# Optimization experiments

Hardware: AMD Instinct MI355X
Metric: run time of the kernel (lower is better)

The kernel has to match this reference:

```python
import jax, jax.numpy as jnp
import numpy as np
import math

B, CIN, H, W = 8, 64, 64, 64
C = 64  # channels (== in_channels, required since conv_out is unused and residual is added raw)
TEMPERATURE = 1.0


def setup_inputs() -> dict:
    key = jax.random.key(0)
    ks = jax.random.split(key, 7)
    s = 1.0 / math.sqrt(CIN)
    return {
        "x": jax.random.normal(ks[0], (B, CIN, H, W), dtype=jnp.float32),
        "wq": jax.random.uniform(ks[1], (C, CIN), jnp.float32, -s, s),
        "bq": jax.random.uniform(ks[2], (C,), jnp.float32, -s, s),
        "wk": jax.random.uniform(ks[3], (C, CIN), jnp.float32, -s, s),
        "bk": jax.random.uniform(ks[4], (C,), jnp.float32, -s, s),
        "wv": jax.random.uniform(ks[5], (C, CIN), jnp.float32, -s, s),
        "bv": jax.random.uniform(ks[6], (C,), jnp.float32, -s, s),
    }


def reference(x, wq, bq, wk, bk, wv, bv):
    b, cin, h, w = x.shape
    n = h * w
    xf = x.reshape(b, cin, n)  # [B,Cin,N]
    # 1x1 convs == per-pixel GEMM
    q = jnp.einsum('oc,bcn->bon', wq, xf) + bq[None, :, None]  # [B,C,N]
    k = jnp.einsum('oc,bcn->bon', wk, xf) + bk[None, :, None]
    v = jnp.einsum('oc,bcn->bon', wv, xf) + bv[None, :, None]
    # 'channel' whitening: subtract per-channel spatial mean
    q_mean = q.mean(axis=2, keepdims=True)  # [B,C,1]
    k_mean = k.mean(axis=2, keepdims=True)
    q = q - q_mean
    k = k - k_mean
    scale = math.sqrt(C)
    # pairwise term: softmax over keys of whitened q.k / (scale*temperature)
    sim = jnp.einsum('bcn,bcm->bnm', q, k) / (scale * TEMPERATURE)  # [B,N,N]
    sim = jax.nn.softmax(sim, axis=2)
    out = jnp.einsum('bnm,bcm->bcn', sim, v)  # [B,C,N]
    # unary term: softmax(query_mean . key) over keys, no scaling (as in source)
    unary = jax.nn.softmax(jnp.einsum('bc,bcm->bm', q_mean[:, :, 0], k), axis=-1)  # [B,N]
    out_unary = jnp.einsum('bcm,bm->bc', v, unary)  # [B,C]
    out = out + out_unary[:, :, None]
    return x + out.reshape(b, C, h, w)
```

## Files before the change

### kernel.cpp

```cpp
#include <hip/hip_runtime.h>
#include <stdint.h>

#define N_PIX 4096
#define NB 8

typedef __attribute__((ext_vector_type(8))) short short8;
typedef __attribute__((ext_vector_type(4))) float f32x4;
typedef __attribute__((ext_vector_type(2))) uint32_t u32x2;

#define SCL 0.18033688011112042f
#define LOG2E 1.4426950408889634f

__device__ __forceinline__ short f2bf(float x){
  union { float f; uint32_t u; } a; a.f = x;
  uint32_t r = a.u + 0x7FFFu + ((a.u >> 16) & 1u);
  return (short)(r >> 16);
}
__device__ __forceinline__ float bf2f(short h){
  union { uint32_t u; float f; } a; a.u = ((uint32_t)(uint16_t)h) << 16; return a.f;
}
__device__ __forceinline__ uint32_t cvtpk(float lo, float hi){
  uint32_t r;
  asm("v_cvt_pk_bf16_f32 %0, %1, %2" : "=v"(r) : "v"(lo), "v"(hi));
  return r;
}
__device__ __forceinline__ float fexp2(float x){ return __builtin_amdgcn_exp2f(x); }
__device__ __forceinline__ float wredSum(float v){
  #pragma unroll
  for (int m = 1; m < 64; m <<= 1) v += __shfl_xor(v, m);
  return v;
}
__device__ __forceinline__ float wredMax(float v){
  #pragma unroll
  for (int m = 1; m < 64; m <<= 1) v = fmaxf(v, __shfl_xor(v, m));
  return v;
}

__global__ __launch_bounds__(256) void k_xmean(const float* __restrict__ x, float* __restrict__ xm){
  int row = blockIdx.x;
  int tid = threadIdx.x;
  const float* xr = x + (size_t)row * N_PIX;
  float s = 0.f;
  #pragma unroll
  for (int i = 0; i < 16; i++) s += xr[tid + 256*i];
  s = wredSum(s);
  __shared__ float red[4];
  if ((tid & 63) == 0) red[tid >> 6] = s;
  __syncthreads();
  if (tid == 0) xm[row] = (red[0]+red[1]+red[2]+red[3]) * (1.0f / N_PIX);
}

__global__ void k_means(const float* __restrict__ wq, const float* __restrict__ bq,
                        const float* __restrict__ wk, const float* __restrict__ bk,
                        const float* __restrict__ xm, float* __restrict__ qm, float* __restrict__ km){
  int b = blockIdx.x; int c = threadIdx.x;
  float sq = 0.f, sk = 0.f;
  for (int cc = 0; cc < 64; cc++){
    float xv = xm[b*64 + cc];
    sq += wq[c*64 + cc] * xv;
    sk += wk[c*64 + cc] * xv;
  }
  qm[b*64 + c] = sq + bq[c];
  km[b*64 + c] = sk + bk[c];
}

__global__ __launch_bounds__(256) void k_qkv(
    const float* __restrict__ x,
    const float* __restrict__ wq, const float* __restrict__ bq,
    const float* __restrict__ wk, const float* __restrict__ bk,
    const float* __restrict__ wv, const float* __restrict__ bv,
    const float* __restrict__ qm, const float* __restrict__ km,
    short* __restrict__ Q, short* __restrict__ Kf, short* __restrict__ Vf,
    float* __restrict__ u)
{
  int blk = blockIdx.x;
  int b  = blk >> 5;
  int n0 = (blk & 31) * 128;
  int tid = threadIdx.x;
  int w = tid >> 6, l = tid & 63, lr = l & 15, lg = l >> 4;
  const float* xb = x + (size_t)b * 64 * N_PIX;

  int ncol[2];
  ncol[0] = n0 + w*32 + lr;
  ncol[1] = ncol[0] + 16;

  short8 bx[2][2];
  #pragma unroll
  for (int tj = 0; tj < 2; tj++){
    #pragma unroll
    for (int kc = 0; kc < 2; kc++){
      short8 t;
      #pragma unroll
      for (int j = 0; j < 8; j++){
        int cp = kc*32 + lg*8 + j;
        t[j] = f2bf(xb[(size_t)cp * N_PIX + ncol[tj]]);
      }
      bx[tj][kc] = t;
    }
  }

  float qmv[4][4];
  #pragma unroll
  for (int ti = 0; ti < 4; ti++)
    #pragma unroll
    for (int r = 0; r < 4; r++)
      qmv[ti][r] = qm[b*64 + ti*16 + lg*4 + r];

  short* Qb  = Q  + (size_t)b * N_PIX * 64;
  short* Kfb = Kf + (size_t)b * N_PIX * 64;
  short* Vfb = Vf + (size_t)b * N_PIX * 64;
  const f32x4 z4 = {0.f, 0.f, 0.f, 0.f};

  {
    short8 aw[4][2];
    #pragma unroll
    for (int ti = 0; ti < 4; ti++)
      #pragma unroll
      for (int kc = 0; kc < 2; kc++){
        const float* wr = wq + (ti*16 + lr)*64 + kc*32 + lg*8;
        short8 t;
        #pragma unroll
        for (int j = 0; j < 8; j++) t[j] = f2bf(wr[j]);
        aw[ti][kc] = t;
      }
    f32x4 acc[4][2];
    #pragma unroll
    for (int ti = 0; ti < 4; ti++)
      #pragma unroll
      for (int tj = 0; tj < 2; tj++){
        acc[ti][tj] = z4;
        #pragma unroll
        for (int kc = 0; kc < 2; kc++)
          acc[ti][tj] = __builtin_amdgcn_mfma_f32_16x16x32_bf16(aw[ti][kc], bx[tj][kc], acc[ti][tj], 0, 0, 0);
      }
    float adj[4][4];
    #pragma unroll
    for (int ti = 0; ti < 4; ti++)
      #pragma unroll
      for (int r = 0; r < 4; r++)
        adj[ti][r] = bq[ti*16 + lg*4 + r] - qmv[ti][r];
    #pragma unroll
    for (int ti = 0; ti < 4; ti++)
      #pragma unroll
      for (int tj = 0; tj < 2; tj++){
        float v0 = (acc[ti][tj][0] + adj[ti][0]) * SCL;
        float v1 = (acc[ti][tj][1] + adj[ti][1]) * SCL;
        float v2 = (acc[ti][tj][2] + adj[ti][2]) * SCL;
        float v3 = (acc[ti][tj][3] + adj[ti][3]) * SCL;
        uint32_t p0 = ((uint32_t)(uint16_t)f2bf(v1) << 16) | (uint16_t)f2bf(v0);
        uint32_t p1 = ((uint32_t)(uint16_t)f2bf(v3) << 16) | (uint16_t)f2bf(v2);
        uint32_t* qr = (uint32_t*)(Qb + (size_t)ncol[tj]*64);
        qr[ti*8 + lg*2]     = p0;
        qr[ti*8 + lg*2 + 1] = p1;
      }
  }

  {
    short8 aw[4][2];
    #pragma unroll
    for (int ti = 0; ti < 4; ti++)
      #pragma unroll
      for (int kc = 0; kc < 2; kc++){
        const float* wr = wk + (ti*16 + lr)*64 + kc*32 + lg*8;
        short8 t;
        #pragma unroll
        for (int j = 0; j < 8; j++) t[j] = f2bf(wr[j]);
        aw[ti][kc] = t;
      }
    f32x4 acc[4][2];
    #pragma unroll
    for (int ti = 0; ti < 4; ti++)
      #pragma unroll
      for (int tj = 0; tj < 2; tj++){
        acc[ti][tj] = z4;
        #pragma unroll
        for (int kc = 0; kc < 2; kc++)
          acc[ti][tj] = __builtin_amdgcn_mfma_f32_16x16x32_bf16(aw[ti][kc], bx[tj][kc], acc[ti][tj], 0, 0, 0);
      }
    float adj[4][4];
    #pragma unroll
    for (int ti = 0; ti < 4; ti++)
      #pragma unroll
      for (int r = 0; r < 4; r++)
        adj[ti][r] = bk[ti*16 + lg*4 + r] - km[b*64 + ti*16 + lg*4 + r];
    float up[2] = {0.f, 0.f};
    #pragma unroll
    for (int ti = 0; ti < 4; ti++)
      #pragma unroll
      for (int tj = 0; tj < 2; tj++){
        float v0 = acc[ti][tj][0] + adj[ti][0];
        float v1 = acc[ti][tj][1] + adj[ti][1];
        float v2 = acc[ti][tj][2] + adj[ti][2];
        float v3 = acc[ti][tj][3] + adj[ti][3];
        up[tj] += qmv[ti][0]*v0 + qmv[ti][1]*v1 + qmv[ti][2]*v2 + qmv[ti][3]*v3;
        uint32_t p0 = ((uint32_t)(uint16_t)f2bf(v1) << 16) | (uint16_t)f2bf(v0);
        uint32_t p1 = ((uint32_t)(uint16_t)f2bf(v3) << 16) | (uint16_t)f2bf(v2);
        int n = ncol[tj];
        int di = (n >> 4)*512 + (ti >> 1)*256
               + ((n & 15) + 16*(2*(ti & 1) + (lg >> 1)))*4 + (lg & 1)*2;
        uint32_t* kr = (uint32_t*)Kfb;
        kr[di]     = p0;
        kr[di + 1] = p1;
      }
    #pragma unroll
    for (int tj = 0; tj < 2; tj++){
      float s = up[tj];
      s += __shfl_xor(s, 16);
      s += __shfl_xor(s, 32);
      if (lg == 0) u[(size_t)b*N_PIX + ncol[tj]] = s;
    }
  }

  {
    short8 aw[4][2];
    #pragma unroll
    for (int ti = 0; ti < 4; ti++)
      #pragma unroll
      for (int kc = 0; kc < 2; kc++){
        const float* wr = wv + (ti*16 + lr)*64 + kc*32 + lg*8;
        short8 t;
        #pragma unroll
        for (int j = 0; j < 8; j++) t[j] = f2bf(wr[j]);
        aw[ti][kc] = t;
      }
    f32x4 acc[4][2];
    #pragma unroll
    for (int ti = 0; ti < 4; ti++)
      #pragma unroll
      for (int tj = 0; tj < 2; tj++){
        acc[ti][tj] = z4;
        #pragma unroll
        for (int kc = 0; kc < 2; kc++)
          acc[ti][tj] = __builtin_amdgcn_mfma_f32_16x16x32_bf16(aw[ti][kc], bx[tj][kc], acc[ti][tj], 0, 0, 0);
      }
    #pragma unroll
    for (int ti = 0; ti < 4; ti++)
      #pragma unroll
      for (int tj = 0; tj < 2; tj++){
        int n = ncol[tj];
        short* vr = Vfb + (n >> 5)*2048 + ti*512 + ((n & 31) >> 3)*128 + (n & 7);
        #pragma unroll
        for (int r = 0; r < 4; r++){
          float v = acc[ti][tj][r] + bv[ti*16 + lg*4 + r];
          vr[(lg*4 + r)*8] = f2bf(v);
        }
      }
  }
}

__global__ __launch_bounds__(256) void k_unary(const float* __restrict__ u, const short* __restrict__ Vf,
                                               float* __restrict__ ou){
  int b = blockIdx.x >> 6, c = blockIdx.x & 63;
  int tid = threadIdx.x, w = tid >> 6, l = tid & 63;
  const float* ub = u + (size_t)b * N_PIX;
  float mx = -1e30f;
  #pragma unroll
  for (int i = 0; i < 16; i++) mx = fmaxf(mx, ub[tid + 256*i]);
  mx = wredMax(mx);
  __shared__ float redm[4];
  if (l == 0) redm[w] = mx;
  __syncthreads();
  mx = fmaxf(fmaxf(redm[0], redm[1]), fmaxf(redm[2], redm[3]));
  const short* Vfb = Vf + (size_t)b * N_PIX * 64;
  int f = c >> 4, lrc = c & 15;
  float ps = 0.f, vs = 0.f;
  #pragma unroll
  for (int i = 0; i < 2; i++){
    int t = i*256 + tid;
    const short8 v = *(const short8*)(Vfb + (t >> 2)*2048 + f*512 + (t & 3)*128 + lrc*8);
    #pragma unroll
    for (int j = 0; j < 8; j++){
      int m = t*8 + j;
      float p = exp2f((ub[m] - mx) * LOG2E);
      ps += p;
      vs += p * bf2f(v[j]);
    }
  }
  ps = wredSum(ps); vs = wredSum(vs);
  __shared__ float r1[4], r2[4];
  if (l == 0){ r1[w] = ps; r2[w] = vs; }
  __syncthreads();
  if (tid == 0) ou[b*64 + c] = (r2[0]+r2[1]+r2[2]+r2[3]) / (r1[0]+r1[1]+r1[2]+r1[3]);
}

__global__ __launch_bounds__(512, 3) void k_attn(
    const short* __restrict__ Q, const short* __restrict__ Kf, const short* __restrict__ Vf,
    const float* __restrict__ ou, const float* __restrict__ x, float* __restrict__ out)
{
  int blk = blockIdx.x;
  int b  = blk & 7;
  int q0 = (blk >> 3) << 6;
  int tid = threadIdx.x;
  int w = tid >> 6, l = tid & 63, lr = l & 15, lg = l >> 4;

  __shared__ char smem[36864];
  short* Pw = (short*)(smem + w*4096);
  short (*Opart)[64][66] = (short(*)[64][66])smem;
  float (*lW)[64] = (float(*)[64])(smem + 34816);

  const short* Qb  = Q  + (size_t)b * N_PIX * 64;
  const short* Kfb = Kf + (size_t)b * N_PIX * 64;
  const short* Vfb = Vf + (size_t)b * N_PIX * 64;

  short8 bq[4][2];
  #pragma unroll
  for (int qt = 0; qt < 4; qt++)
    #pragma unroll
    for (int kc = 0; kc < 2; kc++)
      bq[qt][kc] = *(const short8*)(Qb + (size_t)(q0 + qt*16 + lr)*64 + kc*32 + lg*8);

  f32x4 acc[4][4];
  float rs[4];
  const f32x4 z4 = {0.f, 0.f, 0.f, 0.f};
  #pragma unroll
  for (int qt = 0; qt < 4; qt++){
    rs[qt] = 0.f;
    #pragma unroll
    for (int f = 0; f < 4; f++) acc[qt][f] = z4;
  }

  int kbase = w << 9;
  int sw = (lr & 3) << 4;

  for (int it = 0; it < 16; ++it){
    int kb = kbase + (it << 5);
    const short* kp = Kfb + (size_t)kb * 64 + l*8;
    short8 ak00 = *(const short8*)(kp);
    short8 ak01 = *(const short8*)(kp + 512);
    short8 ak10 = *(const short8*)(kp + 1024);
    short8 ak11 = *(const short8*)(kp + 1536);
    const short* vp = Vfb + (size_t)kb * 64 + l*8;
    short8 bv0 = *(const short8*)(vp);
    short8 bv1 = *(const short8*)(vp + 512);
    short8 bv2 = *(const short8*)(vp + 1024);
    short8 bv3 = *(const short8*)(vp + 1536);

    #pragma unroll
    for (int qt = 0; qt < 4; qt++){
      f32x4 s0 = __builtin_amdgcn_mfma_f32_16x16x32_bf16(ak00, bq[qt][0], z4, 0, 0, 0);
      s0 = __builtin_amdgcn_mfma_f32_16x16x32_bf16(ak01, bq[qt][1], s0, 0, 0, 0);
      f32x4 s1 = __builtin_amdgcn_mfma_f32_16x16x32_bf16(ak10, bq[qt][0], z4, 0, 0, 0);
      s1 = __builtin_amdgcn_mfma_f32_16x16x32_bf16(ak11, bq[qt][1], s1, 0, 0, 0);
      float p00 = fexp2(s0[0]), p01 = fexp2(s0[1]), p02 = fexp2(s0[2]), p03 = fexp2(s0[3]);
      float p10 = fexp2(s1[0]), p11 = fexp2(s1[1]), p12 = fexp2(s1[2]), p13 = fexp2(s1[3]);
      rs[qt] += ((p00 + p01) + (p02 + p03)) + ((p10 + p11) + (p12 + p13));
      u32x2 w0, w1;
      w0[0] = cvtpk(p00, p01); w0[1] = cvtpk(p02, p03);
      w1[0] = cvtpk(p10, p11); w1[1] = cvtpk(p12, p13);
      char* base = (char*)Pw + (qt*16 + lr)*64;
      *(u32x2*)(base + ((lg*8) ^ sw))      = w0;
      *(u32x2*)(base + ((32 + lg*8) ^ sw)) = w1;
    }
    #pragma unroll
    for (int qt = 0; qt < 4; qt++){
      short8 ap = *(const short8*)((char*)Pw + (qt*16 + lr)*64 + ((lg*16) ^ sw));
      acc[qt][0] = __builtin_amdgcn_mfma_f32_16x16x32_bf16(ap, bv0, acc[qt][0], 0, 0, 0);
      acc[qt][1] = __builtin_amdgcn_mfma_f32_16x16x32_bf16(ap, bv1, acc[qt][1], 0, 0, 0);
      acc[qt][2] = __builtin_amdgcn_mfma_f32_16x16x32_bf16(ap, bv2, acc[qt][2], 0, 0, 0);
      acc[qt][3] = __builtin_amdgcn_mfma_f32_16x16x32_bf16(ap, bv3, acc[qt][3], 0, 0, 0);
    }
  }

  #pragma unroll
  for (int qt = 0; qt < 4; qt++){
    float v = rs[qt];
    v += __shfl_xor(v, 16);
    v += __shfl_xor(v, 32);
    rs[qt] = v;
  }

  __syncthreads();

  if (lg == 0){
    #pragma unroll
    for (int qt = 0; qt < 4; qt++)
      lW[w][qt*16 + lr] = rs[qt];
  }
  if (w < 4){
    #pragma unroll
    for (int qt = 0; qt < 4; qt++)
      #pragma unroll
      for (int f = 0; f < 4; f++)
        #pragma unroll
        for (int r = 0; r < 4; r++)
          Opart[w][qt*16 + lg*4 + r][f*16 + lr] = f2bf(acc[qt][f][r]);
  }
  __syncthreads();

  float os[8];
  #pragma unroll
  for (int i = 0; i < 8; i++){
    int idx = i*512 + tid;
    int c = idx >> 6, q = idx & 63;
    os[i] = bf2f(Opart[0][q][c]) + bf2f(Opart[1][q][c])
          + bf2f(Opart[2][q][c]) + bf2f(Opart[3][q][c]);
  }
  __syncthreads();

  if (w >= 4){
    #pragma unroll
    for (int qt = 0; qt < 4; qt++)
      #pragma unroll
      for (int f = 0; f < 4; f++)
        #pragma unroll
        for (int r = 0; r < 4; r++)
          Opart[w-4][qt*16 + lg*4 + r][f*16 + lr] = f2bf(acc[qt][f][r]);
  }
  __syncthreads();

  const float* xb = x + (size_t)b * 64 * N_PIX;
  float* ob = out + (size_t)b * 64 * N_PIX;
  const float* oub = ou + b*64;
  #pragma unroll
  for (int i = 0; i < 8; i++){
    int idx = i*512 + tid;
    int c = idx >> 6, q = idx & 63;
    float o2 = bf2f(Opart[0][q][c]) + bf2f(Opart[1][q][c])
             + bf2f(Opart[2][q][c]) + bf2f(Opart[3][q][c]);
    float lt = lW[0][q] + lW[1][q] + lW[2][q] + lW[3][q]
             + lW[4][q] + lW[5][q] + lW[6][q] + lW[7][q];
    size_t gi = (size_t)c * N_PIX + q0 + q;
    ob[gi] = xb[gi] + (os[i] + o2) / lt + oub[c];
  }
}

extern "C" void kernel_launch(void* const* d_in, const int* in_sizes, int n_in,
                              void* d_out, int out_size, void* d_ws, size_t ws_size,
                              hipStream_t stream)
{
  (void)in_sizes; (void)n_in; (void)out_size; (void)ws_size;
  const float* x  = (const float*)d_in[0];
  const float* wq = (const float*)d_in[1];
  const float* bq = (const float*)d_in[2];
  const float* wk = (const float*)d_in[3];
  const float* bk = (const float*)d_in[4];
  const float* wv = (const float*)d_in[5];
  const float* bv = (const float*)d_in[6];
  float* out = (float*)d_out;

  char* ws = (char*)d_ws;
  short* Q  = (short*)(ws);
  short* Kf = (short*)(ws + 4194304);
  short* Vf = (short*)(ws + 8388608);
  float* u  = (float*)(ws + 12582912);
  float* xm = (float*)(ws + 12713984);
  float* qm = (float*)(ws + 12716032);
  float* km = (float*)(ws + 12718080);
  float* ou = (float*)(ws + 12720128);

  k_xmean<<<dim3(512), dim3(256), 0, stream>>>(x, xm);
  k_means<<<dim3(8), dim3(64), 0, stream>>>(wq, bq, wk, bk, xm, qm, km);
  k_qkv<<<dim3(256), dim3(256), 0, stream>>>(x, wq, bq, wk, bk, wv, bv, qm, km, Q, Kf, Vf, u);
  k_unary<<<dim3(512), dim3(256), 0, stream>>>(u, Vf, ou);
  k_attn<<<dim3(512), dim3(512), 0, stream>>>(Q, Kf, Vf, ou, x, out);
}
```

Before: 79.69 us.

## Permute V layout so P stays in registers for the PV MFMA

Changes how the V projection kernel writes V into its fragment layout, and updates the unary kernel's reads to match. With that permuted key order, the bf16-packed probabilities from the QK MFMA output can be fed straight in as the B operand of the PV MFMA. This removes the per-iteration LDS write and read of P. The epilogue now gives all 8 waves their own Opart buffer, so the reduction happens in one pass with fewer barriers. In exchange the kernel uses more LDS (about 68KB), which may lower how many blocks fit on a CU at the launch bound of 3.

```diff
diff --git a/kernel.cpp b/kernel.cpp
--- a/kernel.cpp
+++ b/kernel.cpp
@@ -238,11 +238,11 @@
       #pragma unroll
       for (int tj = 0; tj < 2; tj++){
         int n = ncol[tj];
-        short* vr = Vfb + (n >> 5)*2048 + ti*512 + ((n & 31) >> 3)*128 + (n & 7);
+        short* vr = Vfb + (n >> 5)*2048 + ti*512 + ((lr >> 2)*16 + lg*4)*8 + (lr & 3) + 4*tj;
         #pragma unroll
         for (int r = 0; r < 4; r++){
           float v = acc[ti][tj][r] + bv[ti*16 + lg*4 + r];
-          vr[(lg*4 + r)*8] = f2bf(v);
+          vr[r*8] = f2bf(v);
         }
       }
   }
@@ -262,15 +262,17 @@
   __syncthreads();
   mx = fmaxf(fmaxf(redm[0], redm[1]), fmaxf(redm[2], redm[3]));
   const short* Vfb = Vf + (size_t)b * N_PIX * 64;
-  int f = c >> 4, lrc = c & 15;
+  int f = c >> 4, c15 = c & 15;
+  int g = tid >> 1, h = tid & 1;
   float ps = 0.f, vs = 0.f;
   #pragma unroll
-  for (int i = 0; i < 2; i++){
-    int t = i*256 + tid;
-    const short8 v = *(const short8*)(Vfb + (t >> 2)*2048 + f*512 + (t & 3)*128 + lrc*8);
+  for (int si = 0; si < 2; si++){
+    int s = 2*h + si;
+    const short8 v = *(const short8*)(Vfb + g*2048 + f*512 + (s*16 + c15)*8);
     #pragma unroll
     for (int j = 0; j < 8; j++){
-      int m = t*8 + j;
+      int kk = (j < 4) ? (4*s + j) : (16 + 4*s + (j - 4));
+      int m = g*32 + kk;
       float p = exp2f((ub[m] - mx) * LOG2E);
       ps += p;
       vs += p * bf2f(v[j]);
@@ -293,10 +295,8 @@
   int tid = threadIdx.x;
   int w = tid >> 6, l = tid & 63, lr = l & 15, lg = l >> 4;
 
-  __shared__ char smem[36864];
-  short* Pw = (short*)(smem + w*4096);
-  short (*Opart)[64][66] = (short(*)[64][66])smem;
-  float (*lW)[64] = (float(*)[64])(smem + 34816);
+  __shared__ short Opart[8][64][66];
+  __shared__ float lW[8][64];
 
   const short* Qb  = Q  + (size_t)b * N_PIX * 64;
   const short* Kfb = Kf + (size_t)b * N_PIX * 64;
@@ -320,7 +320,6 @@
   }
 
   int kbase = w << 9;
-  int sw = (lr & 3) << 4;
 
   for (int it = 0; it < 16; ++it){
     int kb = kbase + (it << 5);
@@ -330,10 +329,10 @@
     short8 ak10 = *(const short8*)(kp + 1024);
     short8 ak11 = *(const short8*)(kp + 1536);
     const short* vp = Vfb + (size_t)kb * 64 + l*8;
-    short8 bv0 = *(const short8*)(vp);
-    short8 bv1 = *(const short8*)(vp + 512);
-    short8 bv2 = *(const short8*)(vp + 1024);
-    short8 bv3 = *(const short8*)(vp + 1536);
+    short8 vf0 = *(const short8*)(vp);
+    short8 vf1 = *(const short8*)(vp + 512);
+    short8 vf2 = *(const short8*)(vp + 1024);
+    short8 vf3 = *(const short8*)(vp + 1536);
 
     #pragma unroll
     for (int qt = 0; qt < 4; qt++){
@@ -344,20 +343,15 @@
       float p00 = fexp2(s0[0]), p01 = fexp2(s0[1]), p02 = fexp2(s0[2]), p03 = fexp2(s0[3]);
       float p10 = fexp2(s1[0]), p11 = fexp2(s1[1]), p12 = fexp2(s1[2]), p13 = fexp2(s1[3]);
       rs[qt] += ((p00 + p01) + (p02 + p03)) + ((p10 + p11) + (p12 + p13));
-      u32x2 w0, w1;
-      w0[0] = cvtpk(p00, p01); w0[1] = cvtpk(p02, p03);
-      w1[0] = cvtpk(p10, p11); w1[1] = cvtpk(p12, p13);
-      char* base = (char*)Pw + (qt*16 + lr)*64;
-      *(u32x2*)(base + ((lg*8) ^ sw))      = w0;
-      *(u32x2*)(base + ((32 + lg*8) ^ sw)) = w1;
-    }
-    #pragma unroll
-    for (int qt = 0; qt < 4; qt++){
-      short8 ap = *(const short8*)((char*)Pw + (qt*16 + lr)*64 + ((lg*16) ^ sw));
-      acc[qt][0] = __builtin_amdgcn_mfma_f32_16x16x32_bf16(ap, bv0, acc[qt][0], 0, 0, 0);
-      acc[qt][1] = __builtin_amdgcn_mfma_f32_16x16x32_bf16(ap, bv1, acc[qt][1], 0, 0, 0);
-      acc[qt][2] = __builtin_amdgcn_mfma_f32_16x16x32_bf16(ap, bv2, acc[qt][2], 0, 0, 0);
-      acc[qt][3] = __builtin_amdgcn_mfma_f32_16x16x32_bf16(ap, bv3, acc[qt][3], 0, 0, 0);
+      union { short8 s; uint32_t u[4]; } pb;
+      pb.u[0] = cvtpk(p00, p01);
+      pb.u[1] = cvtpk(p02, p03);
+      pb.u[2] = cvtpk(p10, p11);
+      pb.u[3] = cvtpk(p12, p13);
+      acc[qt][0] = __builtin_amdgcn_mfma_f32_16x16x32_bf16(vf0, pb.s, acc[qt][0], 0, 0, 0);
+      acc[qt][1] = __builtin_amdgcn_mfma_f32_16x16x32_bf16(vf1, pb.s, acc[qt][1], 0, 0, 0);
+      acc[qt][2] = __builtin_amdgcn_mfma_f32_16x16x32_bf16(vf2, pb.s, acc[qt][2], 0, 0, 0);
+      acc[qt][3] = __builtin_amdgcn_mfma_f32_16x16x32_bf16(vf3, pb.s, acc[qt][3], 0, 0, 0);
     }
   }
 
@@ -369,58 +363,35 @@
     rs[qt] = v;
   }
 
-  __syncthreads();
-
   if (lg == 0){
     #pragma unroll
     for (int qt = 0; qt < 4; qt++)
       lW[w][qt*16 + lr] = rs[qt];
   }
-  if (w < 4){
-    #pragma unroll
-    for (int qt = 0; qt < 4; qt++)
-      #pragma unroll
-      for (int f = 0; f < 4; f++)
-        #pragma unroll
-        for (int r = 0; r < 4; r++)
-          Opart[w][qt*16 + lg*4 + r][f*16 + lr] = f2bf(acc[qt][f][r]);
-  }
+  #pragma unroll
+  for (int qt = 0; qt < 4; qt++)
+    #pragma unroll
+    for (int f = 0; f < 4; f++)
+      #pragma unroll
+      for (int r = 0; r < 4; r++)
+        Opart[w][qt*16 + lr][f*16 + lg*4 + r] = f2bf(acc[qt][f][r]);
   __syncthreads();
 
-  float os[8];
+  const float* xb = x + (size_t)b * 64 * N_PIX;
+  float* ob = out + (size_t)b * 64 * N_PIX;
+  const float* oub = ou + b*64;
   #pragma unroll
   for (int i = 0; i < 8; i++){
     int idx = i*512 + tid;
     int c = idx >> 6, q = idx & 63;
-    os[i] = bf2f(Opart[0][q][c]) + bf2f(Opart[1][q][c])
-          + bf2f(Opart[2][q][c]) + bf2f(Opart[3][q][c]);
-  }
-  __syncthreads();
-
-  if (w >= 4){
-    #pragma unroll
-    for (int qt = 0; qt < 4; qt++)
-      #pragma unroll
-      for (int f = 0; f < 4; f++)
-        #pragma unroll
-        for (int r = 0; r < 4; r++)
-          Opart[w-4][qt*16 + lg*4 + r][f*16 + lr] = f2bf(acc[qt][f][r]);
-  }
-  __syncthreads();
-
-  const float* xb = x + (size_t)b * 64 * N_PIX;
-  float* ob = out + (size_t)b * 64 * N_PIX;
-  const float* oub = ou + b*64;
-  #pragma unroll
-  for (int i = 0; i < 8; i++){
-    int idx = i*512 + tid;
-    int c = idx >> 6, q = idx & 63;
-    float o2 = bf2f(Opart[0][q][c]) + bf2f(Opart[1][q][c])
-             + bf2f(Opart[2][q][c]) + bf2f(Opart[3][q][c]);
-    float lt = lW[0][q] + lW[1][q] + lW[2][q] + lW[3][q]
-             + lW[4][q] + lW[5][q] + lW[6][q] + lW[7][q];
+    float os = 0.f, lt = 0.f;
+    #pragma unroll
+    for (int ww = 0; ww < 8; ww++){
+      os += bf2f(Opart[ww][q][c]);
+      lt += lW[ww][q];
+    }
     size_t gi = (size_t)c * N_PIX + q0 + q;
-    ob[gi] = xb[gi] + (os[i] + o2) / lt + oub[c];
+    ob[gi] = xb[gi] + os / lt + oub[c];
   }
 }
 
```

New measurement: 79.42 us. About the same (-0.3%).
